# Kernel tuning notes

Measured on AMD Instinct MI355X. Metric: run time of the kernel, lower is better.

Reference implementation:

```python
import jax, jax.numpy as jnp
import numpy as np

N_NODES = 50000
N_EDGES = 800000
N_GRAPHS = 64

def _glorot(key, shape, scale=0.05):
    return jax.random.normal(key, shape, dtype=jnp.float32) * scale

def setup_inputs() -> dict:
    key = jax.random.key(0)
    ks = jax.random.split(key, 32)
    inp = {
        'x': jax.random.normal(ks[0], (N_NODES, 17), dtype=jnp.float32),
        'edge_index': jax.random.randint(ks[1], (2, N_EDGES), 0, N_NODES, dtype=jnp.int64) if jax.config.jax_enable_x64 else jax.random.randint(ks[1], (2, N_EDGES), 0, N_NODES).astype(jnp.int32),
        'batch': jnp.sort(jax.random.randint(ks[2], (N_NODES,), 0, N_GRAPHS)),
        'observable_features': jax.random.normal(ks[3], (N_GRAPHS, 5), dtype=jnp.float32),
        'noise_factor': jax.random.uniform(ks[4], (N_GRAPHS, 1), dtype=jnp.float32),
        'noisy_exp': jax.random.normal(ks[5], (N_GRAPHS, 1), dtype=jnp.float32),
        # GATv2 layer 1: 17 -> 128 (heads=1)
        'Wl1': _glorot(ks[6], (17, 128)), 'bl1': jnp.zeros((128,), jnp.float32),
        'Wr1': _glorot(ks[7], (17, 128)), 'br1': jnp.zeros((128,), jnp.float32),
        'att1': _glorot(ks[8], (128,)), 'bias1': jnp.zeros((128,), jnp.float32),
        # GATv2 layer 2: 128 -> 32
        'Wl2': _glorot(ks[9], (128, 32)), 'bl2': jnp.zeros((32,), jnp.float32),
        'Wr2': _glorot(ks[10], (128, 32)), 'br2': jnp.zeros((32,), jnp.float32),
        'att2': _glorot(ks[11], (32,)), 'bias2': jnp.zeros((32,), jnp.float32),
        # obs_encoder: 5 -> 32 -> 8
        'Wo1': _glorot(ks[12], (5, 32)), 'bo1': jnp.zeros((32,), jnp.float32),
        'Wo2': _glorot(ks[13], (32, 8)), 'bo2': jnp.zeros((8,), jnp.float32),
        # noise_encoder: 1 -> 4
        'Wn': _glorot(ks[14], (1, 4)), 'bn': jnp.zeros((4,), jnp.float32),
        # fusion: 45 -> 256 -> 32 -> 1 (dropout inactive at eval)
        'Wf1': _glorot(ks[15], (45, 256)), 'bf1': jnp.zeros((256,), jnp.float32),
        'Wf2': _glorot(ks[16], (256, 32)), 'bf2': jnp.zeros((32,), jnp.float32),
        'Wf3': _glorot(ks[17], (32, 1)), 'bf3': jnp.zeros((1,), jnp.float32),
    }
    return inp

def gatv2_layer(x, src, dst, Wl, bl, Wr, br, att, bias, n_nodes):
    # PyG GATv2Conv, heads=1, concat=True, negative_slope=0.2
    xl = x @ Wl + bl            # source transform  [N, d]
    xr = x @ Wr + br            # target transform  [N, d]
    e = jax.nn.leaky_relu(xl[src] + xr[dst], 0.2)   # [E, d]
    score = e @ att                                   # [E]
    # softmax over incoming edges per target node (stable)
    m = jax.ops.segment_max(score, dst, num_segments=n_nodes)
    ex = jnp.exp(score - m[dst])
    denom = jax.ops.segment_sum(ex, dst, num_segments=n_nodes)
    alpha = ex / (denom[dst] + 1e-16)
    out = jax.ops.segment_sum(alpha[:, None] * xl[src], dst, num_segments=n_nodes)
    return out + bias

def _forward(x, edge_index, batch, observable_features, noise_factor, noisy_exp,
             Wl1, bl1, Wr1, br1, att1, bias1,
             Wl2, bl2, Wr2, br2, att2, bias2,
             Wo1, bo1, Wo2, bo2, Wn, bn,
             Wf1, bf1, Wf2, bf2, Wf3, bf3):
    n = x.shape[0]
    # add self loops (GATv2Conv default add_self_loops=True)
    loops = jnp.arange(n, dtype=edge_index.dtype)
    src = jnp.concatenate([edge_index[0], loops])
    dst = jnp.concatenate([edge_index[1], loops])
    h = jax.nn.elu(gatv2_layer(x, src, dst, Wl1, bl1, Wr1, br1, att1, bias1, n))
    h = jax.nn.elu(gatv2_layer(h, src, dst, Wl2, bl2, Wr2, br2, att2, bias2, n))
    # global mean pool over graphs
    sums = jax.ops.segment_sum(h, batch, num_segments=N_GRAPHS)
    cnts = jax.ops.segment_sum(jnp.ones((n,), h.dtype), batch, num_segments=N_GRAPHS)
    circuit_embedding = sums / jnp.maximum(cnts, 1.0)[:, None]     # [G, 32]
    obs_embedding = jax.nn.relu(observable_features @ Wo1 + bo1) @ Wo2 + bo2  # [G, 8]
    noise_embedding = noise_factor @ Wn + bn                        # [G, 4]
    combined = jnp.concatenate([circuit_embedding, obs_embedding, noise_embedding,
                                noisy_exp.reshape(-1, 1)], axis=1)  # [G, 45]
    hfc = jax.nn.relu(combined @ Wf1 + bf1)
    hfc = jax.nn.relu(hfc @ Wf2 + bf2)
    correction = hfc @ Wf3 + bf3                                    # [G, 1]
    return noisy_exp + correction

def reference(x, edge_index, batch, observable_features, noise_factor, noisy_exp,
              Wl1, bl1, Wr1, br1, att1, bias1,
              Wl2, bl2, Wr2, br2, att2, bias2,
              Wo1, bo1, Wo2, bo2, Wn, bn,
              Wf1, bf1, Wf2, bf2, Wf3, bf3):
    return _forward(x, edge_index, batch, observable_features, noise_factor, noisy_exp,
                    Wl1, bl1, Wr1, br1, att1, bias1,
                    Wl2, bl2, Wr2, br2, att2, bias2,
                    Wo1, bo1, Wo2, bo2, Wn, bn,
                    Wf1, bf1, Wf2, bf2, Wf3, bf3)
```

## Files before the change

### kernel.cpp

```cpp
#include <hip/hip_runtime.h>
#include <math.h>

#define DEV __device__ __forceinline__

typedef __attribute__((ext_vector_type(8))) short bf16x8;
typedef __attribute__((ext_vector_type(4))) float f32x4;
typedef __attribute__((ext_vector_type(2))) float f32x2;

#define CAP 64
#define HB 4

DEV f32x2 pk_add(f32x2 a, f32x2 b) {
    f32x2 d;
    asm("v_pk_add_f32 %0, %1, %2" : "=v"(d) : "v"(a), "v"(b));
    return d;
}
DEV f32x2 pk_fma(f32x2 a, f32x2 b, f32x2 c) {
    f32x2 d;
    asm("v_pk_fma_f32 %0, %1, %2, %3" : "=v"(d) : "v"(a), "v"(b), "v"(c));
    return d;
}

template<int CTRL>
DEV float dpp_add(float x) {
    int y = __builtin_amdgcn_update_dpp(0, __float_as_int(x), CTRL, 0xf, 0xf, true);
    return x + __int_as_float(y);
}
DEV float sum16(float p) {
    p = dpp_add<0x121>(p);
    p = dpp_add<0x122>(p);
    p = dpp_add<0x124>(p);
    p = dpp_add<0x128>(p);
    return p;
}

DEV unsigned short bf16r(float f) {
    unsigned u = __float_as_uint(f);
    return (unsigned short)((u + 0x7FFFu + ((u >> 16) & 1u)) >> 16);
}
DEV unsigned pack_bf16(float a, float b) {
    return (unsigned)bf16r(a) | ((unsigned)bf16r(b) << 16);
}
DEV f32x2 up2(unsigned u) {
    f32x2 v;
    v.x = __uint_as_float(u << 16);
    v.y = __uint_as_float(u & 0xFFFF0000u);
    return v;
}

__global__ void k_zero(int* __restrict__ cnt, int N, float* __restrict__ pooled, int PN) {
    int i = blockIdx.x * blockDim.x + threadIdx.x;
    int s = gridDim.x * blockDim.x;
    for (int j = i; j < N; j += s) cnt[j] = 0;
    for (int j = i; j < PN; j += s) pooled[j] = 0.f;
}

__global__ void __launch_bounds__(256) k_fillx1(
        const int* __restrict__ ei, int E, int ET,
        int* __restrict__ cnt, unsigned short* __restrict__ seg,
        const float* __restrict__ x,
        const float* __restrict__ Wl, const float* __restrict__ bl,
        const float* __restrict__ Wr, const float* __restrict__ br,
        unsigned* __restrict__ xlb, unsigned* __restrict__ xrb, int N, int FB) {
    if (blockIdx.x < FB) {
        int idx = blockIdx.x * blockDim.x + threadIdx.x;
        int stride = FB * blockDim.x;
        int s[HB], d[HB]; bool v[HB];
#pragma unroll
        for (int c = 0; c < HB; c++) {
            int e = idx + c * stride;
            v[c] = e < ET;
            int ee = v[c] ? e : 0;
            s[c] = (ee < E) ? ei[ee] : (ee - E);
            d[c] = (ee < E) ? ei[E + ee] : (ee - E);
        }
        int sl[HB];
#pragma unroll
        for (int c = 0; c < HB; c++)
            sl[c] = v[c] ? atomicAdd(cnt + d[c], 1) : CAP;
#pragma unroll
        for (int c = 0; c < HB; c++)
            if (v[c] && sl[c] < CAP) seg[(size_t)d[c] * CAP + sl[c]] = (unsigned short)s[c];
        return;
    }
    int lane = threadIdx.x & 63;
    int d0 = 2 * lane;
    float wl0[17], wl1[17], wr0[17], wr1[17];
#pragma unroll
    for (int k = 0; k < 17; k++) {
        wl0[k] = Wl[k * 128 + d0];
        wl1[k] = Wl[k * 128 + d0 + 1];
        wr0[k] = Wr[k * 128 + d0];
        wr1[k] = Wr[k * 128 + d0 + 1];
    }
    float bl0 = bl[d0], bl1v = bl[d0 + 1], br0 = br[d0], br1v = br[d0 + 1];
    int xb = blockIdx.x - FB;
    int nxb = gridDim.x - FB;
    int wid = (xb * blockDim.x + threadIdx.x) >> 6;
    int nw = nxb * (blockDim.x >> 6);
    for (int n0 = wid; n0 < N; n0 += nw) {
        int n = __builtin_amdgcn_readfirstlane(n0);
        const float* xp = x + (size_t)n * 17;
        float xk[17];
#pragma unroll
        for (int k = 0; k < 17; k++) xk[k] = xp[k];
        float a0 = bl0, a1 = bl1v, b0 = br0, b1 = br1v;
#pragma unroll
        for (int k = 0; k < 17; k++) {
            a0 = fmaf(xk[k], wl0[k], a0);
            a1 = fmaf(xk[k], wl1[k], a1);
            b0 = fmaf(xk[k], wr0[k], b0);
            b1 = fmaf(xk[k], wr1[k], b1);
        }
        xlb[(size_t)n * 64 + lane] = pack_bf16(a0, a1);
        xrb[(size_t)n * 64 + lane] = pack_bf16(b0, b1);
    }
}

#define CH1 4
__global__ void k_agg1(const int* __restrict__ cnt, const unsigned short* __restrict__ seg,
                       const uint4* __restrict__ xlb, const uint4* __restrict__ xrb,
                       const float* __restrict__ att, const float* __restrict__ bias,
                       uint4* __restrict__ h1b, int N) {
    int node = (blockIdx.x * blockDim.x + threadIdx.x) >> 4;
    int sub = threadIdx.x & 15;
    if (node >= N) return;
    int je = cnt[node];
    if (je > CAP) je = CAP;
    const unsigned short* rowu = seg + (size_t)node * CAP;
    f32x2 r2[4];
    {
        uint4 rv = xrb[node * 16 + sub];
        r2[0] = up2(rv.x); r2[1] = up2(rv.y); r2[2] = up2(rv.z); r2[3] = up2(rv.w);
    }
    const float4* att4 = (const float4*)att;
    float4 aa = att4[sub * 2], ab = att4[sub * 2 + 1];
    f32x2 a6[4], a4[4];
    a6[0].x = 0.6f * aa.x; a6[0].y = 0.6f * aa.y;
    a6[1].x = 0.6f * aa.z; a6[1].y = 0.6f * aa.w;
    a6[2].x = 0.6f * ab.x; a6[2].y = 0.6f * ab.y;
    a6[3].x = 0.6f * ab.z; a6[3].y = 0.6f * ab.w;
    a4[0].x = 0.4f * aa.x; a4[0].y = 0.4f * aa.y;
    a4[1].x = 0.4f * aa.z; a4[1].y = 0.4f * aa.w;
    a4[2].x = 0.4f * ab.x; a4[2].y = 0.4f * ab.y;
    a4[3].x = 0.4f * ab.z; a4[3].y = 0.4f * ab.w;
    f32x2 acc2[4];
#pragma unroll
    for (int j = 0; j < 4; j++) { acc2[j].x = 0.f; acc2[j].y = 0.f; }
    float den = 0.f;
    for (int j0 = 0; j0 < je; j0 += CH1) {
        uint2 sv = *(const uint2*)(rowu + j0);
        int s[CH1];
        s[0] = sv.x & 0xFFFF;
        s[1] = (j0 + 1 < je) ? (int)(sv.x >> 16) : s[0];
        s[2] = (j0 + 2 < je) ? (int)(sv.y & 0xFFFF) : s[0];
        s[3] = (j0 + 3 < je) ? (int)(sv.y >> 16) : s[0];
        uint4 lv[CH1];
        f32x2 l[CH1][4];
        float p[CH1];
#pragma unroll
        for (int c = 0; c < CH1; c++) lv[c] = xlb[s[c] * 16 + sub];
#pragma unroll
        for (int c = 0; c < CH1; c++) {
            l[c][0] = up2(lv[c].x); l[c][1] = up2(lv[c].y);
            l[c][2] = up2(lv[c].z); l[c][3] = up2(lv[c].w);
        }
#pragma unroll
        for (int c = 0; c < CH1; c++) {
            f32x2 q2; q2.x = 0.f; q2.y = 0.f;
#pragma unroll
            for (int j = 0; j < 4; j++) {
                f32x2 v = pk_add(l[c][j], r2[j]);
                f32x2 av;
                av.x = fabsf(v.x); av.y = fabsf(v.y);
                q2 = pk_fma(v, a6[j], q2);
                q2 = pk_fma(av, a4[j], q2);
            }
            p[c] = q2.x + q2.y;
        }
#pragma unroll
        for (int c = 0; c < CH1; c++) p[c] = sum16(p[c]);
#pragma unroll
        for (int c = 0; c < CH1; c++) {
            float e = (j0 + c < je) ? __expf(p[c]) : 0.f;
            den += e;
            f32x2 e2; e2.x = e; e2.y = e;
#pragma unroll
            for (int j = 0; j < 4; j++) acc2[j] = pk_fma(l[c][j], e2, acc2[j]);
        }
    }
    float inv = 1.f / (den + 1e-16f);
    const float4* bias4 = (const float4*)bias;
    float4 b0 = bias4[sub * 2], b1 = bias4[sub * 2 + 1];
    float o[8];
    o[0] = acc2[0].x * inv + b0.x; o[1] = acc2[0].y * inv + b0.y;
    o[2] = acc2[1].x * inv + b0.z; o[3] = acc2[1].y * inv + b0.w;
    o[4] = acc2[2].x * inv + b1.x; o[5] = acc2[2].y * inv + b1.y;
    o[6] = acc2[3].x * inv + b1.z; o[7] = acc2[3].y * inv + b1.w;
#pragma unroll
    for (int d = 0; d < 8; d++) o[d] = (o[d] > 0.f) ? o[d] : expm1f(o[d]);
    uint4 ov;
    ov.x = pack_bf16(o[0], o[1]); ov.y = pack_bf16(o[2], o[3]);
    ov.z = pack_bf16(o[4], o[5]); ov.w = pack_bf16(o[6], o[7]);
    h1b[node * 16 + sub] = ov;
}

__global__ void __launch_bounds__(256) k_xform2(
        const unsigned short* __restrict__ h1b,
        const float* __restrict__ Wl, const float* __restrict__ bl,
        const float* __restrict__ Wr, const float* __restrict__ br,
        unsigned short* __restrict__ xc2, int N) {
    int l = threadIdx.x & 63;
    int m = l & 15;
    int kg = l >> 4;
    bf16x8 w[4][4];
    float bias[4];
#pragma unroll
    for (int dt = 0; dt < 4; dt++) {
        int col = dt * 16 + m;
        const float* W = (col < 32) ? Wl : Wr;
        int c = col & 31;
        bias[dt] = (col < 32) ? bl[c] : br[c];
#pragma unroll
        for (int kc = 0; kc < 4; kc++) {
#pragma unroll
            for (int i = 0; i < 8; i++) {
                int k = kc * 32 + kg * 8 + i;
                w[dt][kc][i] = (short)bf16r(W[k * 32 + c]);
            }
        }
    }
    int ntiles = (N + 15) >> 4;
    int wid = (blockIdx.x * blockDim.x + threadIdx.x) >> 6;
    int nw = gridDim.x * (blockDim.x >> 6);
    for (int tb = wid; tb < ntiles; tb += nw) {
        int arow = tb * 16 + m;
        if (arow >= N) arow = N - 1;
        const bf16x8* ap = (const bf16x8*)(h1b + (size_t)arow * 128);
        f32x4 acc0 = {0.f, 0.f, 0.f, 0.f}, acc1 = acc0, acc2 = acc0, acc3 = acc0;
#pragma unroll
        for (int kc = 0; kc < 4; kc++) {
            bf16x8 a = ap[kc * 4 + kg];
            acc0 = __builtin_amdgcn_mfma_f32_16x16x32_bf16(a, w[0][kc], acc0, 0, 0, 0);
            acc1 = __builtin_amdgcn_mfma_f32_16x16x32_bf16(a, w[1][kc], acc1, 0, 0, 0);
            acc2 = __builtin_amdgcn_mfma_f32_16x16x32_bf16(a, w[2][kc], acc2, 0, 0, 0);
            acc3 = __builtin_amdgcn_mfma_f32_16x16x32_bf16(a, w[3][kc], acc3, 0, 0, 0);
        }
#pragma unroll
        for (int j = 0; j < 4; j++) {
            int orow = tb * 16 + kg * 4 + j;
            if (orow < N) {
                size_t base = (size_t)orow * 64 + m;
                xc2[base]      = bf16r(acc0[j] + bias[0]);
                xc2[base + 16] = bf16r(acc1[j] + bias[1]);
                xc2[base + 32] = bf16r(acc2[j] + bias[2]);
                xc2[base + 48] = bf16r(acc3[j] + bias[3]);
            }
        }
    }
}

#define CH2 8
__global__ void k_agg2(const int* __restrict__ cnt, const unsigned short* __restrict__ seg,
                       const unsigned* __restrict__ xc2,
                       const float* __restrict__ att, const float* __restrict__ bias,
                       float2* __restrict__ h2, int N) {
    int node = (blockIdx.x * blockDim.x + threadIdx.x) >> 4;
    int sub = threadIdx.x & 15;
    if (node >= N) return;
    int je = cnt[node];
    if (je > CAP) je = CAP;
    const unsigned short* rowu = seg + (size_t)node * CAP;
    f32x2 r2 = up2(xc2[node * 32 + 16 + sub]);
    float2 a = reinterpret_cast<const float2*>(att)[sub];
    f32x2 a6, a4;
    a6.x = 0.6f * a.x; a6.y = 0.6f * a.y;
    a4.x = 0.4f * a.x; a4.y = 0.4f * a.y;
    float den = 0.f;
    f32x2 acc; acc.x = 0.f; acc.y = 0.f;
    for (int j0 = 0; j0 < je; j0 += CH2) {
        uint4 sv = *(const uint4*)(rowu + j0);
        int s[CH2];
        s[0] = sv.x & 0xFFFF;
        s[1] = (j0 + 1 < je) ? (int)(sv.x >> 16) : s[0];
        s[2] = (j0 + 2 < je) ? (int)(sv.y & 0xFFFF) : s[0];
        s[3] = (j0 + 3 < je) ? (int)(sv.y >> 16) : s[0];
        s[4] = (j0 + 4 < je) ? (int)(sv.z & 0xFFFF) : s[0];
        s[5] = (j0 + 5 < je) ? (int)(sv.z >> 16) : s[0];
        s[6] = (j0 + 6 < je) ? (int)(sv.w & 0xFFFF) : s[0];
        s[7] = (j0 + 7 < je) ? (int)(sv.w >> 16) : s[0];
        f32x2 l[CH2];
        float p[CH2];
#pragma unroll
        for (int c = 0; c < CH2; c++) l[c] = up2(xc2[s[c] * 32 + sub]);
#pragma unroll
        for (int c = 0; c < CH2; c++) {
            f32x2 v = pk_add(l[c], r2);
            f32x2 av;
            av.x = fabsf(v.x); av.y = fabsf(v.y);
            f32x2 q2; q2.x = 0.f; q2.y = 0.f;
            q2 = pk_fma(v, a6, q2);
            q2 = pk_fma(av, a4, q2);
            p[c] = q2.x + q2.y;
        }
#pragma unroll
        for (int c = 0; c < CH2; c++) p[c] = sum16(p[c]);
#pragma unroll
        for (int c = 0; c < CH2; c++) {
            float e = (j0 + c < je) ? __expf(p[c]) : 0.f;
            den += e;
            f32x2 e2; e2.x = e; e2.y = e;
            acc = pk_fma(l[c], e2, acc);
        }
    }
    float inv = 1.f / (den + 1e-16f);
    float2 b = reinterpret_cast<const float2*>(bias)[sub];
    float2 o;
    o.x = acc.x * inv + b.x; o.x = (o.x > 0.f) ? o.x : expm1f(o.x);
    o.y = acc.y * inv + b.y; o.y = (o.y > 0.f) ? o.y : expm1f(o.y);
    h2[node * 16 + sub] = o;
}

__global__ void k_pool(const float* __restrict__ h2, const int* __restrict__ batch,
                       float* __restrict__ pooled, int N, int G) {
    int gid = (blockIdx.x * blockDim.x + threadIdx.x) >> 5;
    int d = threadIdx.x & 31;
    int r0 = gid * 8;
    if (r0 >= N) return;
    int rend = r0 + 8; if (rend > N) rend = N;
    int gcur = batch[r0];
    float acc = 0.f;
    for (int r = r0; r < rend; r++) {
        int g = batch[r];
        if (g != gcur) {
            atomicAdd(pooled + gcur * 32 + d, acc);
            acc = 0.f;
            gcur = g;
        }
        acc += h2[(size_t)r * 32 + d];
    }
    atomicAdd(pooled + gcur * 32 + d, acc);
}

__global__ void k_head(const float* __restrict__ pooled, const int* __restrict__ batch,
                       int N, int G,
                       const float* __restrict__ obs, const float* __restrict__ nf,
                       const float* __restrict__ ne,
                       const float* __restrict__ Wo1, const float* __restrict__ bo1,
                       const float* __restrict__ Wo2, const float* __restrict__ bo2,
                       const float* __restrict__ Wn, const float* __restrict__ bn,
                       const float* __restrict__ Wf1, const float* __restrict__ bf1,
                       const float* __restrict__ Wf2, const float* __restrict__ bf2,
                       const float* __restrict__ Wf3, const float* __restrict__ bf3,
                       float* __restrict__ out) {
    __shared__ float comb[45];
    __shared__ float ho[32];
    __shared__ float hh1[256];
    __shared__ float hh2[32];
    __shared__ int bounds[2];
    int g = blockIdx.x;
    int t = threadIdx.x;
    if (t < 2) {
        int target = g + t;
        if (target >= G) bounds[t] = N;
        else {
            int lo = 0, hi = N;
            while (lo < hi) {
                int mid = (lo + hi) >> 1;
                if (batch[mid] < target) lo = mid + 1; else hi = mid;
            }
            bounds[t] = lo;
        }
    }
    __syncthreads();
    int s0 = bounds[0], s1 = bounds[1];
    if (t < 32) {
        float c = (float)(s1 - s0);
        c = (c > 1.f) ? c : 1.f;
        comb[t] = pooled[g * 32 + t] / c;
        float a = bo1[t];
#pragma unroll
        for (int k = 0; k < 5; k++) a += obs[g * 5 + k] * Wo1[k * 32 + t];
        ho[t] = (a > 0.f) ? a : 0.f;
    }
    __syncthreads();
    if (t < 8) {
        float a = bo2[t];
#pragma unroll
        for (int k = 0; k < 32; k++) a += ho[k] * Wo2[k * 8 + t];
        comb[32 + t] = a;
    }
    if (t >= 8 && t < 12) {
        int dd = t - 8;
        comb[40 + dd] = nf[g] * Wn[dd] + bn[dd];
    }
    if (t == 12) comb[44] = ne[g];
    __syncthreads();
    {
        float a = bf1[t];
#pragma unroll
        for (int k = 0; k < 45; k++) a += comb[k] * Wf1[k * 256 + t];
        hh1[t] = (a > 0.f) ? a : 0.f;
    }
    __syncthreads();
    if (t < 32) {
        float a = bf2[t];
#pragma unroll
        for (int k = 0; k < 256; k++) a += hh1[k] * Wf2[k * 32 + t];
        hh2[t] = (a > 0.f) ? a : 0.f;
    }
    __syncthreads();
    if (t == 0) {
        float a = bf3[0];
#pragma unroll
        for (int k = 0; k < 32; k++) a += hh2[k] * Wf3[k];
        out[g] = ne[g] + a;
    }
}

extern "C" void kernel_launch(void* const* d_in, const int* in_sizes, int n_in,
                              void* d_out, int out_size, void* d_ws, size_t ws_size,
                              hipStream_t stream) {
    const float* x = (const float*)d_in[0];
    const int* ei = (const int*)d_in[1];
    const int* batch = (const int*)d_in[2];
    const float* obs = (const float*)d_in[3];
    const float* nf = (const float*)d_in[4];
    const float* ne = (const float*)d_in[5];
    const float* Wl1 = (const float*)d_in[6];
    const float* bl1 = (const float*)d_in[7];
    const float* Wr1 = (const float*)d_in[8];
    const float* br1 = (const float*)d_in[9];
    const float* att1 = (const float*)d_in[10];
    const float* bias1 = (const float*)d_in[11];
    const float* Wl2 = (const float*)d_in[12];
    const float* bl2 = (const float*)d_in[13];
    const float* Wr2 = (const float*)d_in[14];
    const float* br2 = (const float*)d_in[15];
    const float* att2 = (const float*)d_in[16];
    const float* bias2 = (const float*)d_in[17];
    const float* Wo1 = (const float*)d_in[18];
    const float* bo1 = (const float*)d_in[19];
    const float* Wo2 = (const float*)d_in[20];
    const float* bo2 = (const float*)d_in[21];
    const float* Wn = (const float*)d_in[22];
    const float* bn = (const float*)d_in[23];
    const float* Wf1 = (const float*)d_in[24];
    const float* bf1 = (const float*)d_in[25];
    const float* Wf2 = (const float*)d_in[26];
    const float* bf2 = (const float*)d_in[27];
    const float* Wf3 = (const float*)d_in[28];
    const float* bf3 = (const float*)d_in[29];

    const int N = in_sizes[0] / 17;
    const int E = in_sizes[1] / 2;
    const int G = in_sizes[3] / 5;
    const int ET = E + N;

    float* ws = (float*)d_ws;
    size_t o = 0;
    unsigned* xlb = (unsigned*)(ws + o); o += (size_t)N * 64;
    unsigned* xrb = (unsigned*)(ws + o); o += (size_t)N * 64;
    unsigned* h1b = (unsigned*)(ws + o); o += (size_t)N * 64;
    unsigned short* seg = (unsigned short*)(ws + o); o += (size_t)N * 32;
    int* cnt = (int*)(ws + o); o += (size_t)N;
    float* pooled = ws + o; o += (size_t)G * 32;
    unsigned short* xc2 = (unsigned short*)xlb;
    float* h2 = (float*)xrb;

    const int FB = (ET + 256 * HB - 1) / (256 * HB);
    const int XB = 512;

    k_zero<<<128, 256, 0, stream>>>(cnt, N, pooled, G * 32);
    k_fillx1<<<FB + XB, 256, 0, stream>>>(ei, E, ET, cnt, seg,
                                          x, Wl1, bl1, Wr1, br1, xlb, xrb, N, FB);

    k_agg1<<<(N * 16 + 255) / 256, 256, 0, stream>>>(cnt, seg, (const uint4*)xlb,
                                                     (const uint4*)xrb, att1, bias1,
                                                     (uint4*)h1b, N);

    k_xform2<<<160, 256, 0, stream>>>((const unsigned short*)h1b, Wl2, bl2, Wr2, br2,
                                      xc2, N);
    k_agg2<<<(N * 16 + 255) / 256, 256, 0, stream>>>(cnt, seg, (const unsigned*)xc2,
                                                     att2, bias2, (float2*)h2, N);

    {
        int ngroups = (N + 7) / 8;
        int nthreads = ngroups * 32;
        k_pool<<<(nthreads + 255) / 256, 256, 0, stream>>>(h2, batch, pooled, N, G);
    }
    k_head<<<G, 256, 0, stream>>>(pooled, batch, N, G, obs, nf, ne,
                                  Wo1, bo1, Wo2, bo2, Wn, bn,
                                  Wf1, bf1, Wf2, bf2, Wf3, bf3,
                                  (float*)d_out);
}
```

Baseline: 164.7 us.

## Split fill and transform kernels and partition edge bucketing by destination range

The combined fill/transform kernel is split into two launches. The fill kernel now assigns each block to one of eight destination-node ranges, and every group scans all edges but only bucket-inserts edges whose destination falls in its range. This keeps the atomics and the segment writes of each group inside a smaller slice of memory, aiming for better cache locality. In exchange, the edge list is read eight times and there is one extra kernel launch, and the transform no longer overlaps with the fill.

After: 155.1 us. -5.9%, faster.

```diff
diff --git a/kernel.cpp b/kernel.cpp
--- a/kernel.cpp
+++ b/kernel.cpp
@@ -55,24 +55,27 @@
     for (int j = i; j < PN; j += s) pooled[j] = 0.f;
 }
 
-__global__ void __launch_bounds__(256) k_fillx1(
+__global__ void __launch_bounds__(256) k_fill(
         const int* __restrict__ ei, int E, int ET,
-        int* __restrict__ cnt, unsigned short* __restrict__ seg,
-        const float* __restrict__ x,
-        const float* __restrict__ Wl, const float* __restrict__ bl,
-        const float* __restrict__ Wr, const float* __restrict__ br,
-        unsigned* __restrict__ xlb, unsigned* __restrict__ xrb, int N, int FB) {
-    if (blockIdx.x < FB) {
-        int idx = blockIdx.x * blockDim.x + threadIdx.x;
-        int stride = FB * blockDim.x;
+        int* __restrict__ cnt, unsigned short* __restrict__ seg, int N) {
+    int g = blockIdx.x & 7;
+    int rank = blockIdx.x >> 3;
+    int bpg = gridDim.x >> 3;
+    int chunk = (N + 7) >> 3;
+    int lo = g * chunk;
+    int hi = lo + chunk; if (hi > N) hi = N;
+    int idx = rank * blockDim.x + threadIdx.x;
+    int stride = bpg * blockDim.x;
+    for (int e0 = idx; e0 < ET; e0 += stride * HB) {
         int s[HB], d[HB]; bool v[HB];
 #pragma unroll
         for (int c = 0; c < HB; c++) {
-            int e = idx + c * stride;
+            int e = e0 + c * stride;
             v[c] = e < ET;
             int ee = v[c] ? e : 0;
             s[c] = (ee < E) ? ei[ee] : (ee - E);
             d[c] = (ee < E) ? ei[E + ee] : (ee - E);
+            v[c] = v[c] && (d[c] >= lo) && (d[c] < hi);
         }
         int sl[HB];
 #pragma unroll
@@ -81,8 +84,14 @@
 #pragma unroll
         for (int c = 0; c < HB; c++)
             if (v[c] && sl[c] < CAP) seg[(size_t)d[c] * CAP + sl[c]] = (unsigned short)s[c];
-        return;
-    }
+    }
+}
+
+__global__ void __launch_bounds__(256) k_xform1(
+        const float* __restrict__ x,
+        const float* __restrict__ Wl, const float* __restrict__ bl,
+        const float* __restrict__ Wr, const float* __restrict__ br,
+        unsigned* __restrict__ xlb, unsigned* __restrict__ xrb, int N) {
     int lane = threadIdx.x & 63;
     int d0 = 2 * lane;
     float wl0[17], wl1[17], wr0[17], wr1[17];
@@ -94,10 +103,8 @@
         wr1[k] = Wr[k * 128 + d0 + 1];
     }
     float bl0 = bl[d0], bl1v = bl[d0 + 1], br0 = br[d0], br1v = br[d0 + 1];
-    int xb = blockIdx.x - FB;
-    int nxb = gridDim.x - FB;
-    int wid = (xb * blockDim.x + threadIdx.x) >> 6;
-    int nw = nxb * (blockDim.x >> 6);
+    int wid = (blockIdx.x * blockDim.x + threadIdx.x) >> 6;
+    int nw = gridDim.x * (blockDim.x >> 6);
     for (int n0 = wid; n0 < N; n0 += nw) {
         int n = __builtin_amdgcn_readfirstlane(n0);
         const float* xp = x + (size_t)n * 17;
@@ -468,13 +475,10 @@
     unsigned short* xc2 = (unsigned short*)xlb;
     float* h2 = (float*)xrb;
 
-    const int FB = (ET + 256 * HB - 1) / (256 * HB);
-    const int XB = 512;
-
     k_zero<<<128, 256, 0, stream>>>(cnt, N, pooled, G * 32);
-    k_fillx1<<<FB + XB, 256, 0, stream>>>(ei, E, ET, cnt, seg,
-                                          x, Wl1, bl1, Wr1, br1, xlb, xrb, N, FB);
-
+    k_fill<<<832, 256, 0, stream>>>(ei, E, ET, cnt, seg, N);
+
+    k_xform1<<<512, 256, 0, stream>>>(x, Wl1, bl1, Wr1, br1, xlb, xrb, N);
     k_agg1<<<(N * 16 + 255) / 256, 256, 0, stream>>>(cnt, seg, (const uint4*)xlb,
                                                      (const uint4*)xrb, att1, bias1,
                                                      (uint4*)h1b, N);
```
